# Kernel optimization log

Measured on AMD Instinct MI355X. Metric: run time of the kernel, lower is better.

Reference implementation:

```python
import jax, jax.numpy as jnp
import numpy as np

NUM_EMBEDDINGS = 4096
EMBEDDING_DIM = 64
COMMITMENT_LOSS_FACTOR = 0.25


def setup_inputs() -> dict:
    key = jax.random.key(0)
    k1, k2 = jax.random.split(key)
    z = jax.random.normal(k1, (16, 64, 64, EMBEDDING_DIM), dtype=jnp.float32)
    init_range = 1.0 / NUM_EMBEDDINGS
    embeddings = jax.random.uniform(
        k2, (NUM_EMBEDDINGS, EMBEDDING_DIM), dtype=jnp.float32,
        minval=-init_range, maxval=init_range)
    return {"z": z, "embeddings": embeddings}


def reference(z, embeddings):
    # z: [B, H, W, D] channels-last latents; embeddings: [K, D] codebook
    B, H, W, D = z.shape
    z_flat = z.reshape(-1, D)  # [N, D]
    # Squared Euclidean distances (argmin-equivalent to cdist p=2, sqrt is monotone)
    d2 = (jnp.sum(z_flat * z_flat, axis=1, keepdims=True)
          - 2.0 * (z_flat @ embeddings.T)
          + jnp.sum(embeddings * embeddings, axis=1))  # [N, K]
    closest = jnp.argmin(d2, axis=1)  # [N]
    quantized = embeddings[closest].reshape(z.shape)  # gather == one_hot @ embeddings
    quantized_indices = closest.reshape(B, H, W)
    # eval-mode forward (no EMA buffer update)
    commitment_loss = jnp.sum((jax.lax.stop_gradient(quantized) - z) ** 2)
    loss = COMMITMENT_LOSS_FACTOR * commitment_loss
    quantized = z + jax.lax.stop_gradient(quantized - z)  # straight-through
    return (quantized.transpose(0, 3, 1, 2),      # [B, D, H, W]
            quantized_indices[:, None, :, :],      # [B, 1, H, W]
            loss)
```

## Files before the change

### kernel.cpp

```cpp
#include <hip/hip_runtime.h>


typedef _Float16 half8 __attribute__((ext_vector_type(8)));
typedef float f32x4 __attribute__((ext_vector_type(4)));

#define NCODES 4096
#define DIM 64
#define NROWS 65536
#define OUT_IDX_OFF 4194304
#define OUT_LOSS_OFF 4259840

#define WS_EHI   0u
#define WS_EE    524288u
#define WS_RLOSS 540672u
#define WS_TU1   802816u
#define WS_TK1   1327104u
#define WS_TU2   1851392u
#define WS_TK23  2375680u
#define WS_TU3   2899968u
#define WS_TU4   3424256u
#define WS_LISTB 3948544u
#define WS_CNTB  4210688u
#define WS_PART  4210944u

__device__ __forceinline__ float pairwise_sumsq64(const float* v) {
    float r[8];
#pragma unroll
    for (int j = 0; j < 8; ++j) r[j] = __fmul_rn(v[j], v[j]);
#pragma unroll
    for (int m = 1; m < 8; ++m) {
#pragma unroll
        for (int j = 0; j < 8; ++j)
            r[j] = __fadd_rn(r[j], __fmul_rn(v[8 * m + j], v[8 * m + j]));
    }
    float s01 = __fadd_rn(r[0], r[1]);
    float s23 = __fadd_rn(r[2], r[3]);
    float s45 = __fadd_rn(r[4], r[5]);
    float s67 = __fadd_rn(r[6], r[7]);
    return __fadd_rn(__fadd_rn(s01, s23), __fadd_rn(s45, s67));
}

__device__ __forceinline__ float exact_d2(const float* __restrict__ emb, int k,
                                          const float* zr, float zz, float eev) {
    const float4* ep = reinterpret_cast<const float4*>(emb + (size_t)k * DIM);
    float da = 0.f;
#pragma unroll
    for (int q = 0; q < 16; ++q) {
        float4 A = ep[q];
        da += A.x * zr[4 * q + 0]; da += A.y * zr[4 * q + 1];
        da += A.z * zr[4 * q + 2]; da += A.w * zr[4 * q + 3];
    }
    return __fadd_rn(__fsub_rn(zz, __fmul_rn(2.0f, da)), eev);
}

__device__ __forceinline__ void gload_lds16(const void* g, void* l) {
    __builtin_amdgcn_global_load_lds(
        (const __attribute__((address_space(1))) unsigned int*)g,
        (__attribute__((address_space(3))) unsigned int*)l, 16, 0, 0);
}

#define WAITVM(n)                                               \
    {                                                           \
        asm volatile("s_waitcnt vmcnt(" #n ")" ::: "memory");   \
        __builtin_amdgcn_sched_barrier(0);                      \
    }

__global__ void vq_prep(const float* __restrict__ emb, _Float16* __restrict__ ehi,
                        float* __restrict__ ee) {
    int k = blockIdx.x * 256 + threadIdx.x;
    float v[DIM];
    const float4* p = reinterpret_cast<const float4*>(emb + (size_t)k * DIM);
#pragma unroll
    for (int i = 0; i < 16; ++i) {
        float4 a = p[i];
        v[4 * i + 0] = a.x; v[4 * i + 1] = a.y; v[4 * i + 2] = a.z; v[4 * i + 3] = a.w;
    }
    ee[k] = pairwise_sumsq64(v);
#pragma unroll
    for (int i = 0; i < 8; ++i) {
        half8 h;
#pragma unroll
        for (int j = 0; j < 8; ++j) h[j] = (_Float16)(v[8 * i + j] * 256.0f);
        *reinterpret_cast<half8*>(ehi + (size_t)k * DIM + 8 * i) = h;
    }
}

#define INS4MAX(x, xid, s)                                    \
    {                                                         \
        bool q1 = (x) > M1[s], q2 = (x) > M2[s], q3 = (x) > M3[s]; \
        M4[s] = q3 ? M3[s] : fmaxf((x), M4[s]);               \
        M3[s] = q2 ? M2[s] : (q3 ? (x) : M3[s]);              \
        G3[s] = q2 ? G2[s] : (q3 ? (xid) : G3[s]);            \
        M2[s] = q1 ? M1[s] : (q2 ? (x) : M2[s]);              \
        G2[s] = q1 ? G1[s] : (q2 ? (xid) : G2[s]);            \
        M1[s] = q1 ? (x) : M1[s];                             \
        G1[s] = q1 ? (xid) : G1[s];                           \
    }

__launch_bounds__(256, 4)
__global__ void vq_scan(const float* __restrict__ z, const _Float16* __restrict__ ehi,
                        float* __restrict__ tU1, int* __restrict__ tK1,
                        float* __restrict__ tU2, int* __restrict__ tK23,
                        float* __restrict__ tU3, float* __restrict__ tU4) {
    __shared__ float4 sB[4][512];

    const int tid = threadIdx.x;
    const int lane = tid & 63;
    const int w = tid >> 6;
    const int rlo = lane & 15;
    const int quad = lane >> 4;
    const int half = blockIdx.y;
    const int rowbase = blockIdx.x * 128 + w * 32;

    half8 zhi[2][2];
#pragma unroll
    for (int rt = 0; rt < 2; ++rt) {
        const float* zp = z + (size_t)(rowbase + rt * 16 + rlo) * DIM + quad * 8;
#pragma unroll
        for (int ks = 0; ks < 2; ++ks) {
            float4 a = *reinterpret_cast<const float4*>(zp + ks * 32);
            float4 b = *reinterpret_cast<const float4*>(zp + ks * 32 + 4);
            float f[8] = {a.x, a.y, a.z, a.w, b.x, b.y, b.z, b.w};
            half8 hi;
#pragma unroll
            for (int e = 0; e < 8; ++e) hi[e] = (_Float16)f[e];
            zhi[rt][ks] = hi;
        }
    }

    int gOff[2];
#pragma unroll
    for (int i = 0; i < 2; ++i) {
        int L = tid + i * 256;
        int T = L >> 6, u = L & 63;
        int code = (T >> 1) * 16 + (u & 15);
        int dg = (T & 1) * 4 + (u >> 4);
        gOff[i] = (code * 8 + dg) * 16;
    }
    const char* srcHiB = (const char*)ehi + (size_t)half * 2048 * 128;

    auto issue = [&](int cc, int bb) {
        const char* hs = srcHiB + (size_t)cc * 8192;
        char* dH = (char*)&sB[bb][0];
#pragma unroll
        for (int i = 0; i < 2; ++i)
            gload_lds16(hs + gOff[i], dH + (tid + i * 256) * 16);
    };

    issue(0, 0);
    issue(1, 1);

    float M1[2], M2[2], M3[2], M4[2];
    int G1[2], G2[2], G3[2];
#pragma unroll
    for (int s = 0; s < 2; ++s) {
        M1[s] = -3e38f; M2[s] = -3e38f; M3[s] = -3e38f; M4[s] = -3e38f;
        G1[s] = 0; G2[s] = 0; G3[s] = 0;
    }
    const f32x4 zero4 = {0.f, 0.f, 0.f, 0.f};

#pragma unroll 1
    for (int c = 0; c < 32; ++c) {
        if (c < 30) {
            issue(c + 2, (c + 2) & 3);
            WAITVM(4);
        } else if (c == 30) {
            WAITVM(2);
        } else {
            WAITVM(0);
        }
        __builtin_amdgcn_s_barrier();
        __builtin_amdgcn_sched_barrier(0);

        const float4* bh = sB[c & 3];
        float run[2];
#pragma unroll
        for (int s = 0; s < 2; ++s) run[s] = -3e38f;
#pragma unroll
        for (int t = 0; t < 4; ++t) {
            half8 a0h = __builtin_bit_cast(half8, bh[(t * 2 + 0) * 64 + lane]);
            half8 a1h = __builtin_bit_cast(half8, bh[(t * 2 + 1) * 64 + lane]);
#pragma unroll
            for (int rt = 0; rt < 2; ++rt) {
                f32x4 acc = __builtin_amdgcn_mfma_f32_16x16x32_f16(a0h, zhi[rt][0], zero4, 0, 0, 0);
                acc = __builtin_amdgcn_mfma_f32_16x16x32_f16(a1h, zhi[rt][1], acc, 0, 0, 0);
                run[rt] = fmaxf(run[rt],
                                fmaxf(fmaxf(acc[0], acc[1]), fmaxf(acc[2], acc[3])));
            }
        }
        const int gb = (c << 6) + (quad << 2);
#pragma unroll
        for (int s = 0; s < 2; ++s) INS4MAX(run[s], gb, s);
        __builtin_amdgcn_sched_barrier(0);
    }

#pragma unroll
    for (int s = 0; s < 2; ++s) {
#pragma unroll
        for (int d = 16; d < 64; d <<= 1) {
            float o1 = __shfl_xor(M1[s], d); int p1 = __shfl_xor(G1[s], d);
            float o2 = __shfl_xor(M2[s], d); int p2 = __shfl_xor(G2[s], d);
            float o3 = __shfl_xor(M3[s], d); int p3 = __shfl_xor(G3[s], d);
            float o4 = __shfl_xor(M4[s], d);
            INS4MAX(o1, p1, s);
            INS4MAX(o2, p2, s);
            INS4MAX(o3, p3, s);
            M4[s] = fmaxf(M4[s], o4);
        }
    }

    if (lane < 16) {
        const int hoff = half << 11;
#pragma unroll
        for (int s = 0; s < 2; ++s) {
            int grow = rowbase + s * 16 + lane;
            size_t idx = (size_t)half * NROWS + grow;
            tU1[idx] = M1[s] * -0.0078125f;
            tU2[idx] = M2[s] * -0.0078125f;
            tU3[idx] = M3[s] * -0.0078125f;
            tU4[idx] = M4[s] * -0.0078125f;
            tK1[idx] = G1[s] + hoff;
            tK23[idx] = (G2[s] + hoff) | ((G3[s] + hoff) << 16);
        }
    }
}

__global__ void vq_finish(const float* __restrict__ z, const float* __restrict__ emb,
                          const float* __restrict__ ee,
                          const float* __restrict__ tU1, const int* __restrict__ tK1,
                          const float* __restrict__ tU2, const int* __restrict__ tK23,
                          const float* __restrict__ tU3, const float* __restrict__ tU4,
                          float* __restrict__ out,
                          int* __restrict__ listB, int* __restrict__ cntB) {
    const int tid = threadIdx.x;
    const int grp = tid >> 4;
    const int j = tid & 15;
    const int row = blockIdx.x * 16 + grp;

    float u1 = tU1[row]; int g1 = tK1[row];
    float u2 = tU2[row];
    float u3 = tU3[row]; float u4 = tU4[row];
    int k23 = tK23[row];
    int g2 = k23 & 0xFFFF, g3 = ((unsigned)k23) >> 16;
    {
        float b1 = tU1[NROWS + row]; int h1 = tK1[NROWS + row];
        float b2 = tU2[NROWS + row];
        float b3 = tU3[NROWS + row]; float b4 = tU4[NROWS + row];
        int hk = tK23[NROWS + row];
        int h2 = hk & 0xFFFF, h3 = ((unsigned)hk) >> 16;
#define INSU(bv, bi)                                           \
        { bool q1 = (bv) < u1, q2 = (bv) < u2, q3 = (bv) < u3; \
          u4 = q3 ? u3 : fminf((bv), u4);                      \
          u3 = q2 ? u2 : (q3 ? (bv) : u3);                     \
          g3 = q2 ? g2 : (q3 ? (bi) : g3);                     \
          u2 = q1 ? u1 : (q2 ? (bv) : u2);                     \
          g2 = q1 ? g1 : (q2 ? (bi) : g2);                     \
          u1 = q1 ? (bv) : u1;                                 \
          g1 = q1 ? (bi) : g1; }
        INSU(b1, h1);
        INSU(b2, h2);
        INSU(b3, h3);
        u4 = fminf(u4, b4);
#undef INSU
    }

    float zr[DIM];
    {
        const float4* zp = reinterpret_cast<const float4*>(z + (size_t)row * DIM);
#pragma unroll
        for (int i = 0; i < 16; ++i) {
            float4 a = zp[i];
            zr[4 * i + 0] = a.x; zr[4 * i + 1] = a.y; zr[4 * i + 2] = a.z; zr[4 * i + 3] = a.w;
        }
    }
    float zzs = 0.f;
#pragma unroll
    for (int i = 0; i < DIM; ++i) zzs = fmaf(zr[i], zr[i], zzs);

    float delta = ((zzs > 120.f) ? 3.4e-5f : 1.7e-5f) + 2.5e-5f;

    if (j == 0 && u4 - u1 < delta) {
        int p = atomicAdd(cntB, 1);
        listB[p] = row;
    }

    const float zz = pairwise_sumsq64(zr);
    const int joff = ((j >> 2) << 4) + (j & 3);
    unsigned long long bestkey = ~0ull;
    int secs[3]; int nsec = 1; secs[0] = g1;
    if (u2 - u1 < delta) {
        secs[1] = g2; nsec = 2;
        if (u3 - u1 < delta) { secs[2] = g3; nsec = 3; }
    }
    for (int si = 0; si < nsec; ++si) {
        int k = secs[si] + joff;
        float d2 = exact_d2(emb, k, zr, zz, ee[k]);
        unsigned long long key =
            (((unsigned long long)__float_as_uint(d2)) << 32) | (unsigned)k;
        bestkey = key < bestkey ? key : bestkey;
    }
    {
#pragma unroll
        for (int d = 1; d < 16; d <<= 1) {
            unsigned long long o = __shfl_xor(bestkey, d);
            bestkey = o < bestkey ? o : bestkey;
        }
    }
    if (j == 0) out[OUT_IDX_OFF + row] = (float)(int)(bestkey & 0xFFFFFFFFu);
}

__launch_bounds__(256, 4)
__global__ void vq_emit(const float* __restrict__ z, const float* __restrict__ emb,
                        float* __restrict__ out, float* __restrict__ rowloss,
                        double* __restrict__ part) {
    __shared__ float zs[64 * 65];
    __shared__ float qs[64 * 65];
    __shared__ float ls[64 * 5];
    const int tid = threadIdx.x;
    const int rl = tid >> 2;
    const int j = tid & 3;
    const int row = blockIdx.x * 64 + rl;

    {
        const float4* zp = reinterpret_cast<const float4*>(
            z + (size_t)blockIdx.x * 4096 + (size_t)tid * 16);
        float4 a = zp[0], b = zp[1], c = zp[2], d = zp[3];
        float v[16] = {a.x, a.y, a.z, a.w, b.x, b.y, b.z, b.w,
                       c.x, c.y, c.z, c.w, d.x, d.y, d.z, d.w};
        float* dst = &zs[rl * 65 + j * 16];
#pragma unroll
        for (int i = 0; i < 16; ++i) dst[i] = v[i];
    }
    {
        const int kb = (int)out[OUT_IDX_OFF + row];
        const float4* qp = reinterpret_cast<const float4*>(
            emb + (size_t)kb * DIM + j * 16);
        float4 a = qp[0], b = qp[1], c = qp[2], d = qp[3];
        float v[16] = {a.x, a.y, a.z, a.w, b.x, b.y, b.z, b.w,
                       c.x, c.y, c.z, c.w, d.x, d.y, d.z, d.w};
        float* dst = &qs[rl * 65 + j * 16];
#pragma unroll
        for (int i = 0; i < 16; ++i) dst[i] = v[i];
    }
    __syncthreads();

    const int hw_l = tid & 63;
    const int w = tid >> 6;
    const int bimg = row >> 12;
    const int hwb = (blockIdx.x * 64) & 4095;
    float* ob = out + (size_t)bimg * 262144 + hwb + hw_l;
    float lp = 0.f;
#pragma unroll
    for (int k = 0; k < 16; ++k) {
        const int d = w * 16 + k;
        float qv = qs[hw_l * 65 + d];
        float zv = zs[hw_l * 65 + d];
        float df = qv - zv;
        lp = fmaf(df, df, lp);
        ob[(size_t)d * 4096] = qv;
    }
    ls[hw_l * 5 + w] = lp;
    __syncthreads();

    if (tid < 64) {
        float r01 = ls[tid * 5 + 0] + ls[tid * 5 + 1];
        float r23 = ls[tid * 5 + 2] + ls[tid * 5 + 3];
        float rsum = r01 + r23;
        rowloss[blockIdx.x * 64 + tid] = rsum;
        double s = (double)rsum;
#pragma unroll
        for (int d = 1; d < 64; d <<= 1) s += __shfl_xor(s, d);
        if (tid == 0) atomicAdd(&part[blockIdx.x >> 2], s);
    }
}

__global__ void vq_fallback(const float* __restrict__ z, const float* __restrict__ emb,
                            const float* __restrict__ ee, const int* __restrict__ listB,
                            const int* __restrict__ cntB, float* __restrict__ out,
                            const float* __restrict__ rowloss, double* __restrict__ part) {
    __shared__ float sZ[DIM];
    __shared__ unsigned long long sK[4];
    __shared__ int sKb;
    const int n = *cntB;
    const int tid = threadIdx.x;
    const int lane = tid & 63;
    const int w = tid >> 6;

    for (int i = blockIdx.x; i < n; i += 1024) {
        const int row = listB[i];
        __syncthreads();
        if (tid < DIM) sZ[tid] = z[(size_t)row * DIM + tid];
        __syncthreads();
        float zr[DIM];
#pragma unroll
        for (int q = 0; q < DIM; ++q) zr[q] = sZ[q];
        const float zz = pairwise_sumsq64(zr);

        unsigned long long best = ~0ull;
#pragma unroll 1
        for (int j = 0; j < 16; ++j) {
            int c = tid + j * 256;
            float d2 = exact_d2(emb, c, zr, zz, ee[c]);
            unsigned long long key =
                (((unsigned long long)__float_as_uint(d2)) << 32) | (unsigned)c;
            best = key < best ? key : best;
        }
#pragma unroll
        for (int d = 1; d < 64; d <<= 1) {
            unsigned long long o2 = __shfl_xor(best, d);
            best = o2 < best ? o2 : best;
        }
        if (lane == 0) sK[w] = best;
        __syncthreads();
        if (tid == 0) {
            unsigned long long b = sK[0];
            b = sK[1] < b ? sK[1] : b;
            b = sK[2] < b ? sK[2] : b;
            b = sK[3] < b ? sK[3] : b;
            sKb = (int)(b & 0xFFFFFFFFu);
        }
        __syncthreads();
        const int kb = sKb;
        if (tid < DIM) {
            const float qv = emb[(size_t)kb * DIM + tid];
            const float zv = sZ[tid];
            int bimg = row >> 12, hw = row & 4095;
            out[(size_t)bimg * 262144 + (size_t)tid * 4096 + hw] = qv;
            float lp = (qv - zv) * (qv - zv);
#pragma unroll
            for (int d = 1; d < 64; d <<= 1) lp += __shfl_xor(lp, d);
            if (tid == 0) {
                double dl = (double)lp - (double)rowloss[row];
                atomicAdd(&part[row >> 8], dl);
                out[OUT_IDX_OFF + row] = (float)kb;
            }
        }
    }
}

__global__ void vq_red2(const double* __restrict__ part, float* __restrict__ out_loss) {
    __shared__ double sd[256];
    sd[threadIdx.x] = part[threadIdx.x];
    __syncthreads();
    for (int st = 128; st > 0; st >>= 1) {
        if (threadIdx.x < st) sd[threadIdx.x] += sd[threadIdx.x + st];
        __syncthreads();
    }
    if (threadIdx.x == 0) out_loss[0] = (float)(0.25 * sd[0]);
}

extern "C" void kernel_launch(void* const* d_in, const int* in_sizes, int n_in,
                              void* d_out, int out_size, void* d_ws, size_t ws_size,
                              hipStream_t stream) {
    const float* z = (const float*)d_in[0];
    const float* emb = (const float*)d_in[1];
    float* out = (float*)d_out;
    char* ws = (char*)d_ws;

    _Float16* ehi = (_Float16*)(ws + WS_EHI);
    float* ee = (float*)(ws + WS_EE);
    float* rowloss = (float*)(ws + WS_RLOSS);
    float* tU1 = (float*)(ws + WS_TU1);
    int*   tK1 = (int*)(ws + WS_TK1);
    float* tU2 = (float*)(ws + WS_TU2);
    int*   tK23 = (int*)(ws + WS_TK23);
    float* tU3 = (float*)(ws + WS_TU3);
    float* tU4 = (float*)(ws + WS_TU4);
    int* listB = (int*)(ws + WS_LISTB);
    int* cntB  = (int*)(ws + WS_CNTB);
    double* part = (double*)(ws + WS_PART);

    hipMemsetAsync(cntB, 0, sizeof(int), stream);
    hipMemsetAsync(part, 0, 256 * sizeof(double), stream);
    vq_prep<<<NCODES / 256, 256, 0, stream>>>(emb, ehi, ee);
    vq_scan<<<dim3(NROWS / 128, 2), 256, 0, stream>>>(z, ehi, tU1, tK1, tU2, tK23, tU3, tU4);
    vq_finish<<<NROWS / 16, 256, 0, stream>>>(z, emb, ee, tU1, tK1, tU2, tK23, tU3, tU4,
                                              out, listB, cntB);
    vq_emit<<<NROWS / 64, 256, 0, stream>>>(z, emb, out, rowloss, part);
    vq_fallback<<<1024, 256, 0, stream>>>(z, emb, ee, listB, cntB, out, rowloss, part);
    vq_red2<<<1, 256, 0, stream>>>(part, out + OUT_LOSS_OFF);
}
```

Before: 179.8 us.

## Double scan chunk per barrier with 3-stage LDS ring; fold memsets into prep

```diff
diff --git a/kernel.cpp b/kernel.cpp
--- a/kernel.cpp
+++ b/kernel.cpp
@@ -66,7 +66,12 @@
     }
 
 __global__ void vq_prep(const float* __restrict__ emb, _Float16* __restrict__ ehi,
-                        float* __restrict__ ee) {
+                        float* __restrict__ ee, int* __restrict__ cntB,
+                        double* __restrict__ part) {
+    if (blockIdx.x == 0) {
+        part[threadIdx.x] = 0.0;
+        if (threadIdx.x == 0) *cntB = 0;
+    }
     int k = blockIdx.x * 256 + threadIdx.x;
     float v[DIM];
     const float4* p = reinterpret_cast<const float4*>(emb + (size_t)k * DIM);
@@ -102,7 +107,7 @@
                         float* __restrict__ tU1, int* __restrict__ tK1,
                         float* __restrict__ tU2, int* __restrict__ tK23,
                         float* __restrict__ tU3, float* __restrict__ tU4) {
-    __shared__ float4 sB[4][512];
+    __shared__ float4 sB[3][1024];
 
     const int tid = threadIdx.x;
     const int lane = tid & 63;
@@ -128,22 +133,24 @@
         }
     }
 
-    int gOff[2];
-#pragma unroll
-    for (int i = 0; i < 2; ++i) {
+    int gOff[4];
+#pragma unroll
+    for (int i = 0; i < 4; ++i) {
         int L = tid + i * 256;
-        int T = L >> 6, u = L & 63;
+        int ch = L >> 9;
+        int Lc = L & 511;
+        int T = Lc >> 6, u = Lc & 63;
         int code = (T >> 1) * 16 + (u & 15);
         int dg = (T & 1) * 4 + (u >> 4);
-        gOff[i] = (code * 8 + dg) * 16;
+        gOff[i] = ch * 8192 + (code * 8 + dg) * 16;
     }
     const char* srcHiB = (const char*)ehi + (size_t)half * 2048 * 128;
 
-    auto issue = [&](int cc, int bb) {
-        const char* hs = srcHiB + (size_t)cc * 8192;
+    auto issue = [&](int pr, int bb) {
+        const char* hs = srcHiB + (size_t)pr * 16384;
         char* dH = (char*)&sB[bb][0];
 #pragma unroll
-        for (int i = 0; i < 2; ++i)
+        for (int i = 0; i < 4; ++i)
             gload_lds16(hs + gOff[i], dH + (tid + i * 256) * 16);
     };
 
@@ -160,37 +167,39 @@
     const f32x4 zero4 = {0.f, 0.f, 0.f, 0.f};
 
 #pragma unroll 1
-    for (int c = 0; c < 32; ++c) {
-        if (c < 30) {
-            issue(c + 2, (c + 2) & 3);
+    for (int it = 0; it < 16; ++it) {
+        if (it < 15) {
             WAITVM(4);
-        } else if (c == 30) {
-            WAITVM(2);
         } else {
             WAITVM(0);
         }
         __builtin_amdgcn_s_barrier();
         __builtin_amdgcn_sched_barrier(0);
-
-        const float4* bh = sB[c & 3];
-        float run[2];
-#pragma unroll
-        for (int s = 0; s < 2; ++s) run[s] = -3e38f;
-#pragma unroll
-        for (int t = 0; t < 4; ++t) {
-            half8 a0h = __builtin_bit_cast(half8, bh[(t * 2 + 0) * 64 + lane]);
-            half8 a1h = __builtin_bit_cast(half8, bh[(t * 2 + 1) * 64 + lane]);
-#pragma unroll
-            for (int rt = 0; rt < 2; ++rt) {
-                f32x4 acc = __builtin_amdgcn_mfma_f32_16x16x32_f16(a0h, zhi[rt][0], zero4, 0, 0, 0);
-                acc = __builtin_amdgcn_mfma_f32_16x16x32_f16(a1h, zhi[rt][1], acc, 0, 0, 0);
-                run[rt] = fmaxf(run[rt],
-                                fmaxf(fmaxf(acc[0], acc[1]), fmaxf(acc[2], acc[3])));
+        if (it < 14) issue(it + 2, (it + 2) % 3);
+
+        const float4* bp = &sB[it % 3][0];
+#pragma unroll
+        for (int sc = 0; sc < 2; ++sc) {
+            const float4* bh = bp + sc * 512;
+            float run[2];
+#pragma unroll
+            for (int s = 0; s < 2; ++s) run[s] = -3e38f;
+#pragma unroll
+            for (int t = 0; t < 4; ++t) {
+                half8 a0h = __builtin_bit_cast(half8, bh[(t * 2 + 0) * 64 + lane]);
+                half8 a1h = __builtin_bit_cast(half8, bh[(t * 2 + 1) * 64 + lane]);
+#pragma unroll
+                for (int rt = 0; rt < 2; ++rt) {
+                    f32x4 acc = __builtin_amdgcn_mfma_f32_16x16x32_f16(a0h, zhi[rt][0], zero4, 0, 0, 0);
+                    acc = __builtin_amdgcn_mfma_f32_16x16x32_f16(a1h, zhi[rt][1], acc, 0, 0, 0);
+                    run[rt] = fmaxf(run[rt],
+                                    fmaxf(fmaxf(acc[0], acc[1]), fmaxf(acc[2], acc[3])));
+                }
             }
-        }
-        const int gb = (c << 6) + (quad << 2);
-#pragma unroll
-        for (int s = 0; s < 2; ++s) INS4MAX(run[s], gb, s);
+            const int gb = (((it << 1) + sc) << 6) + (quad << 2);
+#pragma unroll
+            for (int s = 0; s < 2; ++s) INS4MAX(run[s], gb, s);
+        }
         __builtin_amdgcn_sched_barrier(0);
     }
 
@@ -470,9 +479,7 @@
     int* cntB  = (int*)(ws + WS_CNTB);
     double* part = (double*)(ws + WS_PART);
 
-    hipMemsetAsync(cntB, 0, sizeof(int), stream);
-    hipMemsetAsync(part, 0, 256 * sizeof(double), stream);
-    vq_prep<<<NCODES / 256, 256, 0, stream>>>(emb, ehi, ee);
+    vq_prep<<<NCODES / 256, 256, 0, stream>>>(emb, ehi, ee, cntB, part);
     vq_scan<<<dim3(NROWS / 128, 2), 256, 0, stream>>>(z, ehi, tU1, tK1, tU2, tK23, tU3, tU4);
     vq_finish<<<NROWS / 16, 256, 0, stream>>>(z, emb, ee, tU1, tK1, tU2, tK23, tU3, tU4,
                                               out, listB, cntB);
```

Result: slower. 183.5 us (+2.1%).
